# Performance work log

Measured on AMD Instinct MI355X. Metric: run time of the kernel, lower is better.

The kernel has to match this reference:

```python
import jax, jax.numpy as jnp
import numpy as np

E = 1024  # embed_dim

def setup_inputs() -> dict:
    key = jax.random.key(0)
    ks = jax.random.split(key, 7)
    s = 1.0 / np.sqrt(E)  # torch Linear default init scale (uniform bound)
    x = jax.random.normal(ks[0], (4, 2048, E), dtype=jnp.float32)
    Wq = jax.random.uniform(ks[1], (E, E), jnp.float32, -s, s)
    bq = jax.random.uniform(ks[2], (E,), jnp.float32, -s, s)
    Wk = jax.random.uniform(ks[3], (E, E), jnp.float32, -s, s)
    bk = jax.random.uniform(ks[4], (E,), jnp.float32, -s, s)
    Wv = jax.random.uniform(ks[5], (E, E), jnp.float32, -s, s)
    bv = jax.random.uniform(ks[6], (E,), jnp.float32, -s, s)
    return {"x": x, "Wq": Wq, "bq": bq, "Wk": Wk, "bk": bk, "Wv": Wv, "bv": bv}

def reference(x, Wq, bq, Wk, bk, Wv, bv):
    # torch nn.Linear: y = x @ W.T + b
    Q = jnp.einsum('bse,fe->bsf', x, Wq) + bq
    K = jnp.einsum('bse,fe->bsf', x, Wk) + bk
    V = jnp.einsum('bse,fe->bsf', x, Wv) + bv
    scale = jnp.sqrt(jnp.asarray(E, x.dtype))
    scores = jnp.einsum('bqd,bkd->bqk', Q, K) / scale  # [B,S,S]
    attn = jax.nn.softmax(scores, axis=-1)
    return jnp.einsum('bqk,bkd->bqd', attn, V)
```

## Files before the change

kernel.cpp:

```cpp
#include <hip/hip_runtime.h>
#include <hip/hip_bf16.h>


typedef __attribute__((ext_vector_type(8))) short bf16x8;
typedef __attribute__((ext_vector_type(4))) float f32x4;

#define DEVI static __device__ __forceinline__

DEVI short to_bf16(float f) {
    unsigned u = __builtin_bit_cast(unsigned, f);
    u += 0x7fffu + ((u >> 16) & 1u);
    return (short)(u >> 16);
}
DEVI float from_bf16(short s) {
    return __builtin_bit_cast(float, (unsigned)((unsigned short)s) << 16);
}

DEVI void gload_lds16(const short* g, short* l) {
    __builtin_amdgcn_global_load_lds(
        (const __attribute__((address_space(1))) void*)g,
        (__attribute__((address_space(3))) void*)l, 16, 0, 0);
}

template<int BM, int BN, int BIAS, typename TOUT>
__global__ __launch_bounds__(256, 2)
void gemm8(const short* __restrict__ A, long lda, long bsA,
           const short* __restrict__ B, long ldb, long bsB,
           const float* __restrict__ b0, const float* __restrict__ b1,
           const float* __restrict__ b2,
           TOUT* __restrict__ c0, TOUT* __restrict__ c1, TOUT* __restrict__ c2,
           long ldc, long bsC, int K, float scale)
{
    constexpr int MF = BM / 16;
    constexpr int NF = BN / 64;
    constexpr int RA = (BM * 32) / (8 * 256);
    constexpr int RB = (BN * 32) / (8 * 256);

    __shared__ __align__(16) short As[3 * BM * 32];
    __shared__ __align__(16) short Bs[3 * BN * 32];

    const int tid = threadIdx.x;
    const int z = blockIdx.z;
    const long m0 = (long)blockIdx.y * BM;
    const long n0 = (long)blockIdx.x * BN;
    const short* Ab = A + (long)z * bsA + m0 * lda;
    const short* Bb = B + (long)z * bsB + n0 * ldb;

    const int wn = tid >> 6;
    const int lane = tid & 63;
    const int lrow = lane & 15;
    const int q = lane >> 4;

    const int NT = K >> 5;

    auto stage = [&](int t, int b) {
        const long koff = (long)t * 32;
        #pragma unroll
        for (int i = 0; i < RA; ++i) {
            int s = i * 256 + tid;
            int row = s >> 2;
            int c = (s & 3) ^ ((row >> 1) & 3);
            gload_lds16(Ab + (long)row * lda + koff + c * 8,
                        &As[b * BM * 32 + s * 8]);
        }
        #pragma unroll
        for (int i = 0; i < RB; ++i) {
            int s = i * 256 + tid;
            int row = s >> 2;
            int c = (s & 3) ^ ((row >> 1) & 3);
            gload_lds16(Bb + (long)row * ldb + koff + c * 8,
                        &Bs[b * BN * 32 + s * 8]);
        }
    };

    f32x4 acc[MF][NF] = {};

    stage(0, 0);
    stage(1, 1);
    asm volatile("s_waitcnt vmcnt(6)" ::: "memory");
    __builtin_amdgcn_sched_barrier(0);
    __builtin_amdgcn_s_barrier();

    int b = 0;
    for (int t = 0; t < NT; ++t) {
        const short* Asb = &As[b * BM * 32];
        const short* Bsb = &Bs[b * BN * 32];

        bf16x8 bfr[NF];
        #pragma unroll
        for (int n = 0; n < NF; ++n) {
            int row = wn * 64 + n * 16 + lrow;
            int p = q ^ ((row >> 1) & 3);
            bfr[n] = *(const bf16x8*)&Bsb[row * 32 + p * 8];
        }
        bf16x8 af[MF];
        #pragma unroll
        for (int m = 0; m < MF; ++m) {
            int row = m * 16 + lrow;
            int p = q ^ ((row >> 1) & 3);
            af[m] = *(const bf16x8*)&Asb[row * 32 + p * 8];
        }

        if (t + 2 < NT) {
            int tb = b + 2; if (tb >= 3) tb -= 3;
            stage(t + 2, tb);
        }

        __builtin_amdgcn_s_setprio(1);
        #pragma unroll
        for (int m = 0; m < MF; ++m)
            #pragma unroll
            for (int n = 0; n < NF; ++n)
                acc[m][n] = __builtin_amdgcn_mfma_f32_16x16x32_bf16(
                    af[m], bfr[n], acc[m][n], 0, 0, 0);
        __builtin_amdgcn_s_setprio(0);

        if (t < NT - 1) {
            asm volatile("s_waitcnt lgkmcnt(0)" ::: "memory");
            asm volatile("s_waitcnt vmcnt(6)" ::: "memory");
            __builtin_amdgcn_sched_barrier(0);
            __builtin_amdgcn_s_barrier();
        }
        ++b; if (b == 3) b = 0;
    }

    const float* bias = (z == 0) ? b0 : (z == 1) ? b1 : b2;
    TOUT* Cz = ((z == 0) ? c0 : (z == 1) ? c1 : c2) + (long)z * bsC;
    TOUT* Cb = Cz + m0 * ldc + n0;
    #pragma unroll
    for (int m = 0; m < MF; ++m) {
        #pragma unroll
        for (int n = 0; n < NF; ++n) {
            #pragma unroll
            for (int r = 0; r < 4; ++r) {
                int row = m * 16 + q * 4 + r;
                int col = wn * 64 + n * 16 + lrow;
                float v = acc[m][n][r] * scale;
                if constexpr (BIAS == 1) v += bias[n0 + col];
                if constexpr (sizeof(TOUT) == 2)
                    Cb[(long)row * ldc + col] = to_bf16(v);
                else
                    Cb[(long)row * ldc + col] = v;
            }
        }
    }
}

__global__ __launch_bounds__(256)
void cvt_f32_bf16(const float* __restrict__ src, short* __restrict__ dst, int n8)
{
    int i = blockIdx.x * 256 + threadIdx.x;
    if (i < n8) {
        float4 a = ((const float4*)src)[2 * i];
        float4 b = ((const float4*)src)[2 * i + 1];
        bf16x8 o = { to_bf16(a.x), to_bf16(a.y), to_bf16(a.z), to_bf16(a.w),
                     to_bf16(b.x), to_bf16(b.y), to_bf16(b.z), to_bf16(b.w) };
        *(bf16x8*)&dst[i * 8] = o;
    }
}

__global__ __launch_bounds__(256)
void cvt3_f32_bf16(const float* __restrict__ s0, const float* __restrict__ s1,
                   const float* __restrict__ s2, short* __restrict__ dst, int n8)
{
    int zz = blockIdx.y;
    const float* src = (zz == 0) ? s0 : (zz == 1) ? s1 : s2;
    int i = blockIdx.x * 256 + threadIdx.x;
    if (i < n8) {
        float4 a = ((const float4*)src)[2 * i];
        float4 b = ((const float4*)src)[2 * i + 1];
        bf16x8 o = { to_bf16(a.x), to_bf16(a.y), to_bf16(a.z), to_bf16(a.w),
                     to_bf16(b.x), to_bf16(b.y), to_bf16(b.z), to_bf16(b.w) };
        *(bf16x8*)&dst[(long)zz * n8 * 8 + i * 8] = o;
    }
}

__global__ __launch_bounds__(256)
void softmax_rows(short* __restrict__ S, int ncols)
{
    const long row = blockIdx.x;
    short* p = S + row * (long)ncols;
    const int t = threadIdx.x;

    union { bf16x8 v; short s[8]; } u;
    u.v = *(const bf16x8*)&p[t * 8];
    float f[8];
    float m = -3.0e38f;
    #pragma unroll
    for (int j = 0; j < 8; ++j) { f[j] = from_bf16(u.s[j]); m = fmaxf(m, f[j]); }
    #pragma unroll
    for (int off = 32; off > 0; off >>= 1) m = fmaxf(m, __shfl_xor(m, off));

    __shared__ float red[8];
    const int wave = t >> 6;
    if ((t & 63) == 0) red[wave] = m;
    __syncthreads();
    m = fmaxf(fmaxf(red[0], red[1]), fmaxf(red[2], red[3]));

    float sum = 0.f;
    #pragma unroll
    for (int j = 0; j < 8; ++j) { f[j] = __expf(f[j] - m); sum += f[j]; }
    #pragma unroll
    for (int off = 32; off > 0; off >>= 1) sum += __shfl_xor(sum, off);
    if ((t & 63) == 0) red[4 + wave] = sum;
    __syncthreads();
    sum = red[4] + red[5] + red[6] + red[7];

    const float inv = 1.0f / sum;
    #pragma unroll
    for (int j = 0; j < 8; ++j) u.s[j] = to_bf16(f[j] * inv);
    *(bf16x8*)&p[t * 8] = u.v;
}

__global__ __launch_bounds__(256)
void transpose_bf16(const short* __restrict__ src, short* __restrict__ dst, int R, int Cc)
{
    __shared__ short tl[32][33];
    const long zoff = (long)blockIdx.z * R * Cc;
    const int r0 = blockIdx.x * 32;
    const int c0 = blockIdx.y * 32;
    const int tid = threadIdx.x;
    #pragma unroll
    for (int i = 0; i < 4; ++i) {
        int qq = tid + 256 * i;
        int r = qq >> 5, c = qq & 31;
        tl[r][c] = src[zoff + (long)(r0 + r) * Cc + c0 + c];
    }
    __syncthreads();
    #pragma unroll
    for (int i = 0; i < 4; ++i) {
        int qq = tid + 256 * i;
        int r = qq >> 5, c = qq & 31;
        dst[zoff + (long)(c0 + r) * R + r0 + c] = tl[c][r];
    }
}

extern "C" void kernel_launch(void* const* d_in, const int* in_sizes, int n_in,
                              void* d_out, int out_size, void* d_ws, size_t ws_size,
                              hipStream_t stream)
{
    (void)in_sizes; (void)n_in; (void)out_size; (void)ws_size;

    const float* x  = (const float*)d_in[0];
    const float* Wq = (const float*)d_in[1];
    const float* bq = (const float*)d_in[2];
    const float* Wk = (const float*)d_in[3];
    const float* bk = (const float*)d_in[4];
    const float* Wv = (const float*)d_in[5];
    const float* bv = (const float*)d_in[6];

    const int S = 2048, E = 1024;
    const long M1 = 1024l * 1024;

    short* w  = (short*)d_ws;
    short* Q  = w;
    short* Kb = w + 8 * M1;
    short* P  = w + 16 * M1;
    short* V  = w + 16 * M1;
    float* out_ws = (float*)w;

    short* dows = (short*)d_out;
    short* xb = dows;
    short* Wb = dows + 8 * M1;
    short* VT = dows;

    dim3 blk(256);

    cvt_f32_bf16<<<dim3(4096), blk, 0, stream>>>(x, xb, (int)M1);
    cvt3_f32_bf16<<<dim3(512, 3), blk, 0, stream>>>(Wq, Wk, Wv, Wb, (int)(M1 / 8));

    gemm8<128, 256, 1, short><<<dim3(4, 64, 3), blk, 0, stream>>>(
        xb, E, 0, Wb, E, M1, bq, bk, bv, Q, Kb, V, E, 0, E, 1.0f);

    transpose_bf16<<<dim3(S / 32, E / 32, 4), blk, 0, stream>>>(V, VT, S, E);

    gemm8<128, 256, 0, short><<<dim3(8, 16, 4), blk, 0, stream>>>(
        Q, E, 2 * M1, Kb, E, 2 * M1, nullptr, nullptr, nullptr,
        P, P, P, S, 4 * M1, E, 0.03125f);

    softmax_rows<<<dim3(4 * S), blk, 0, stream>>>(P, S);

    gemm8<128, 256, 0, float><<<dim3(4, 16, 4), blk, 0, stream>>>(
        P, S, 4 * M1, VT, S, 2 * M1, nullptr, nullptr, nullptr,
        out_ws, out_ws, out_ws, E, 2 * M1, S, 1.0f);

    hipMemcpyAsync(d_out, out_ws, 32l * 1024 * 1024,
                   hipMemcpyDeviceToDevice, stream);
}
```

Baseline: 201.7 us.

## Move GEMMs to 512-thread 256x256 tiles with phased MFMA and reordered buffers

Result: faster. 190.6 us (-5.5%).

```diff
diff --git a/kernel.cpp b/kernel.cpp
--- a/kernel.cpp
+++ b/kernel.cpp
@@ -22,19 +22,20 @@
         (__attribute__((address_space(3))) void*)l, 16, 0, 0);
 }
 
-template<int BM, int BN, int BIAS, typename TOUT>
-__global__ __launch_bounds__(256, 2)
-void gemm8(const short* __restrict__ A, long lda, long bsA,
+template<int BM, int BN, int WARPS_M, int WARPS_N, int BIAS, typename TOUT>
+__global__ __launch_bounds__(512, 2)
+void gemmP(const short* __restrict__ A, long lda, long bsA,
            const short* __restrict__ B, long ldb, long bsB,
            const float* __restrict__ b0, const float* __restrict__ b1,
            const float* __restrict__ b2,
            TOUT* __restrict__ c0, TOUT* __restrict__ c1, TOUT* __restrict__ c2,
            long ldc, long bsC, int K, float scale)
 {
-    constexpr int MF = BM / 16;
-    constexpr int NF = BN / 64;
-    constexpr int RA = (BM * 32) / (8 * 256);
-    constexpr int RB = (BN * 32) / (8 * 256);
+    constexpr int WM = BM / WARPS_M, WN = BN / WARPS_N;
+    constexpr int MF = WM / 16, NF = WN / 16;
+    constexpr int NPH = (MF * NF) / 16;
+    constexpr int PH_MF = MF / NPH;
+    constexpr int RA = BM / 128, RB = BN / 128, LT = RA + RB;
 
     __shared__ __align__(16) short As[3 * BM * 32];
     __shared__ __align__(16) short Bs[3 * BN * 32];
@@ -46,38 +47,44 @@
     const short* Ab = A + (long)z * bsA + m0 * lda;
     const short* Bb = B + (long)z * bsB + n0 * ldb;
 
-    const int wn = tid >> 6;
+    const int wv = tid >> 6;
+    const int wm = wv / WARPS_N;
+    const int wnn = wv % WARPS_N;
     const int lane = tid & 63;
     const int lrow = lane & 15;
     const int q = lane >> 4;
 
     const int NT = K >> 5;
 
-    auto stage = [&](int t, int b) {
+    auto stageA = [&](int t, int bb) {
         const long koff = (long)t * 32;
         #pragma unroll
         for (int i = 0; i < RA; ++i) {
-            int s = i * 256 + tid;
+            int s = i * 512 + tid;
             int row = s >> 2;
             int c = (s & 3) ^ ((row >> 1) & 3);
             gload_lds16(Ab + (long)row * lda + koff + c * 8,
-                        &As[b * BM * 32 + s * 8]);
-        }
+                        &As[bb * BM * 32 + s * 8]);
+        }
+    };
+    auto stageB = [&](int t, int bb) {
+        const long koff = (long)t * 32;
         #pragma unroll
         for (int i = 0; i < RB; ++i) {
-            int s = i * 256 + tid;
+            int s = i * 512 + tid;
             int row = s >> 2;
             int c = (s & 3) ^ ((row >> 1) & 3);
             gload_lds16(Bb + (long)row * ldb + koff + c * 8,
-                        &Bs[b * BN * 32 + s * 8]);
+                        &Bs[bb * BN * 32 + s * 8]);
         }
     };
 
     f32x4 acc[MF][NF] = {};
 
-    stage(0, 0);
-    stage(1, 1);
-    asm volatile("s_waitcnt vmcnt(6)" ::: "memory");
+    stageA(0, 0); stageB(0, 0);
+    stageA(1, 1); stageB(1, 1);
+    if constexpr (LT == 3) asm volatile("s_waitcnt vmcnt(3)" ::: "memory");
+    else                   asm volatile("s_waitcnt vmcnt(4)" ::: "memory");
     __builtin_amdgcn_sched_barrier(0);
     __builtin_amdgcn_s_barrier();
 
@@ -85,39 +92,53 @@
     for (int t = 0; t < NT; ++t) {
         const short* Asb = &As[b * BM * 32];
         const short* Bsb = &Bs[b * BN * 32];
+        int b2 = b + 2; if (b2 >= 3) b2 -= 3;
+        const bool pre = (t + 2 < NT);
 
         bf16x8 bfr[NF];
         #pragma unroll
-        for (int n = 0; n < NF; ++n) {
-            int row = wn * 64 + n * 16 + lrow;
-            int p = q ^ ((row >> 1) & 3);
-            bfr[n] = *(const bf16x8*)&Bsb[row * 32 + p * 8];
-        }
-        bf16x8 af[MF];
-        #pragma unroll
-        for (int m = 0; m < MF; ++m) {
-            int row = m * 16 + lrow;
-            int p = q ^ ((row >> 1) & 3);
-            af[m] = *(const bf16x8*)&Asb[row * 32 + p * 8];
-        }
-
-        if (t + 2 < NT) {
-            int tb = b + 2; if (tb >= 3) tb -= 3;
-            stage(t + 2, tb);
-        }
-
-        __builtin_amdgcn_s_setprio(1);
-        #pragma unroll
-        for (int m = 0; m < MF; ++m)
+        for (int p = 0; p < NPH; ++p) {
+            if (p == 0) {
+                #pragma unroll
+                for (int n = 0; n < NF; ++n) {
+                    int row = wnn * WN + n * 16 + lrow;
+                    int c = q ^ ((row >> 1) & 3);
+                    bfr[n] = *(const bf16x8*)&Bsb[row * 32 + c * 8];
+                }
+            }
+            bf16x8 af[PH_MF];
             #pragma unroll
-            for (int n = 0; n < NF; ++n)
-                acc[m][n] = __builtin_amdgcn_mfma_f32_16x16x32_bf16(
-                    af[m], bfr[n], acc[m][n], 0, 0, 0);
-        __builtin_amdgcn_s_setprio(0);
+            for (int m = 0; m < PH_MF; ++m) {
+                int row = wm * WM + (p * PH_MF + m) * 16 + lrow;
+                int c = q ^ ((row >> 1) & 3);
+                af[m] = *(const bf16x8*)&Asb[row * 32 + c * 8];
+            }
+            if (pre) {
+                if (p == 0) stageA(t + 2, b2);
+                if (p == NPH - 1) stageB(t + 2, b2);
+            }
+            __builtin_amdgcn_s_barrier();
+            asm volatile("s_waitcnt lgkmcnt(0)" ::: "memory");
+            __builtin_amdgcn_sched_barrier(0);
+            __builtin_amdgcn_s_setprio(1);
+            #pragma unroll
+            for (int m = 0; m < PH_MF; ++m)
+                #pragma unroll
+                for (int n = 0; n < NF; ++n)
+                    acc[p * PH_MF + m][n] =
+                        __builtin_amdgcn_mfma_f32_16x16x32_bf16(
+                            af[m], bfr[n], acc[p * PH_MF + m][n], 0, 0, 0);
+            __builtin_amdgcn_s_setprio(0);
+            if (p < NPH - 1) __builtin_amdgcn_s_barrier();
+        }
 
         if (t < NT - 1) {
-            asm volatile("s_waitcnt lgkmcnt(0)" ::: "memory");
-            asm volatile("s_waitcnt vmcnt(6)" ::: "memory");
+            if (pre) {
+                if constexpr (LT == 3) asm volatile("s_waitcnt vmcnt(3)" ::: "memory");
+                else                   asm volatile("s_waitcnt vmcnt(4)" ::: "memory");
+            } else {
+                asm volatile("s_waitcnt vmcnt(0)" ::: "memory");
+            }
             __builtin_amdgcn_sched_barrier(0);
             __builtin_amdgcn_s_barrier();
         }
@@ -133,8 +154,8 @@
         for (int n = 0; n < NF; ++n) {
             #pragma unroll
             for (int r = 0; r < 4; ++r) {
-                int row = m * 16 + q * 4 + r;
-                int col = wn * 64 + n * 16 + lrow;
+                int row = wm * WM + m * 16 + q * 4 + r;
+                int col = wnn * WN + n * 16 + lrow;
                 float v = acc[m][n][r] * scale;
                 if constexpr (BIAS == 1) v += bias[n0 + col];
                 if constexpr (sizeof(TOUT) == 2)
@@ -248,6 +269,7 @@
     const float* bk = (const float*)d_in[4];
     const float* Wv = (const float*)d_in[5];
     const float* bv = (const float*)d_in[6];
+    float* out = (float*)d_out;
 
     const int S = 2048, E = 1024;
     const long M1 = 1024l * 1024;
@@ -256,34 +278,34 @@
     short* Q  = w;
     short* Kb = w + 8 * M1;
     short* P  = w + 16 * M1;
-    short* V  = w + 16 * M1;
-    float* out_ws = (float*)w;
+    short* V  = w;
+    short* VT = w + 8 * M1;
 
     short* dows = (short*)d_out;
     short* xb = dows;
     short* Wb = dows + 8 * M1;
-    short* VT = dows;
-
-    dim3 blk(256);
+
+    dim3 blk(256), blkg(512);
 
     cvt_f32_bf16<<<dim3(4096), blk, 0, stream>>>(x, xb, (int)M1);
     cvt3_f32_bf16<<<dim3(512, 3), blk, 0, stream>>>(Wq, Wk, Wv, Wb, (int)(M1 / 8));
 
-    gemm8<128, 256, 1, short><<<dim3(4, 64, 3), blk, 0, stream>>>(
-        xb, E, 0, Wb, E, M1, bq, bk, bv, Q, Kb, V, E, 0, E, 1.0f);
-
-    transpose_bf16<<<dim3(S / 32, E / 32, 4), blk, 0, stream>>>(V, VT, S, E);
-
-    gemm8<128, 256, 0, short><<<dim3(8, 16, 4), blk, 0, stream>>>(
+    gemmP<256, 256, 2, 4, 1, short><<<dim3(4, 32, 2), blkg, 0, stream>>>(
+        xb, E, 0, Wb, E, M1, bq, bk, nullptr, Q, Kb, nullptr, E, 0, E, 1.0f);
+
+    gemmP<256, 256, 2, 4, 0, short><<<dim3(8, 8, 4), blkg, 0, stream>>>(
         Q, E, 2 * M1, Kb, E, 2 * M1, nullptr, nullptr, nullptr,
         P, P, P, S, 4 * M1, E, 0.03125f);
 
+    gemmP<128, 256, 2, 4, 1, short><<<dim3(4, 64, 1), blkg, 0, stream>>>(
+        xb, E, 0, Wb + 2 * M1, E, 0, bv, nullptr, nullptr,
+        V, nullptr, nullptr, E, 0, E, 1.0f);
+
+    transpose_bf16<<<dim3(S / 32, E / 32, 4), blk, 0, stream>>>(V, VT, S, E);
+
     softmax_rows<<<dim3(4 * S), blk, 0, stream>>>(P, S);
 
-    gemm8<128, 256, 0, float><<<dim3(4, 16, 4), blk, 0, stream>>>(
+    gemmP<128, 256, 2, 4, 0, float><<<dim3(4, 16, 4), blkg, 0, stream>>>(
         P, S, 4 * M1, VT, S, 2 * M1, nullptr, nullptr, nullptr,
-        out_ws, out_ws, out_ws, E, 2 * M1, S, 1.0f);
-
-    hipMemcpyAsync(d_out, out_ws, 32l * 1024 * 1024,
-                   hipMemcpyDeviceToDevice, stream);
-}
+        out, out, out, E, 2 * M1, S, 1.0f);
+}
```

## Rewrite GEMM as 512-thread 256x128 tile kernel and drop final output copy

Applied to the files above, without the earlier changes.

Measured after the change: 225.0 us. 11.5% more time.

```diff
diff --git a/kernel.cpp b/kernel.cpp
--- a/kernel.cpp
+++ b/kernel.cpp
@@ -22,119 +22,148 @@
         (__attribute__((address_space(3))) void*)l, 16, 0, 0);
 }
 
-template<int BM, int BN, int BIAS, typename TOUT>
-__global__ __launch_bounds__(256, 2)
-void gemm8(const short* __restrict__ A, long lda, long bsA,
+template<int BIAS, typename TOUT>
+__global__ __launch_bounds__(512, 2)
+void gemmW(const short* __restrict__ A, long lda, long bsA,
            const short* __restrict__ B, long ldb, long bsB,
-           const float* __restrict__ b0, const float* __restrict__ b1,
-           const float* __restrict__ b2,
+           const float* __restrict__ bi0, const float* __restrict__ bi1,
+           const float* __restrict__ bi2,
            TOUT* __restrict__ c0, TOUT* __restrict__ c1, TOUT* __restrict__ c2,
-           long ldc, long bsC, int K, float scale)
-{
-    constexpr int MF = BM / 16;
-    constexpr int NF = BN / 64;
-    constexpr int RA = (BM * 32) / (8 * 256);
-    constexpr int RB = (BN * 32) / (8 * 256);
-
-    __shared__ __align__(16) short As[3 * BM * 32];
-    __shared__ __align__(16) short Bs[3 * BN * 32];
+           long ldc, long bsC, int K, float scale, int gx)
+{
+    __shared__ __align__(16) short As[3 * 16384];
+    __shared__ __align__(16) short Bs[3 * 8192];
 
     const int tid = threadIdx.x;
-    const int z = blockIdx.z;
-    const long m0 = (long)blockIdx.y * BM;
-    const long n0 = (long)blockIdx.x * BN;
+    const int z = blockIdx.y;
+
+    const int nwg = gridDim.x;
+    const int id = blockIdx.x;
+    const int id2 = (id & 7) * (nwg >> 3) + (id >> 3);
+    const long m0 = (long)(id2 / gx) * 256;
+    const long n0 = (long)(id2 % gx) * 128;
+
     const short* Ab = A + (long)z * bsA + m0 * lda;
     const short* Bb = B + (long)z * bsB + n0 * ldb;
 
-    const int wn = tid >> 6;
+    const int wv = tid >> 6;
+    const int wm = wv >> 2;
+    const int wn = wv & 3;
     const int lane = tid & 63;
     const int lrow = lane & 15;
     const int q = lane >> 4;
 
-    const int NT = K >> 5;
-
-    auto stage = [&](int t, int b) {
-        const long koff = (long)t * 32;
-        #pragma unroll
-        for (int i = 0; i < RA; ++i) {
-            int s = i * 256 + tid;
-            int row = s >> 2;
-            int c = (s & 3) ^ ((row >> 1) & 3);
-            gload_lds16(Ab + (long)row * lda + koff + c * 8,
-                        &As[b * BM * 32 + s * 8]);
-        }
-        #pragma unroll
-        for (int i = 0; i < RB; ++i) {
-            int s = i * 256 + tid;
-            int row = s >> 2;
-            int c = (s & 3) ^ ((row >> 1) & 3);
-            gload_lds16(Bb + (long)row * ldb + koff + c * 8,
-                        &Bs[b * BN * 32 + s * 8]);
-        }
-    };
-
-    f32x4 acc[MF][NF] = {};
-
-    stage(0, 0);
-    stage(1, 1);
+    const int NT = K >> 6;
+
+    auto stA = [&](int t, int bb, int h) {
+        const long k0 = (long)t * 64;
+        #pragma unroll
+        for (int i = 0; i < 2; ++i) {
+            int s = i * 512 + tid;
+            int row = s >> 3, cc = s & 7;
+            int src = cc ^ (row & 7);
+            gload_lds16(Ab + (long)(h * 128 + row) * lda + k0 + src * 8,
+                        &As[bb * 16384 + h * 8192 + s * 8]);
+        }
+    };
+    auto stB = [&](int t, int bb) {
+        const long k0 = (long)t * 64;
+        #pragma unroll
+        for (int i = 0; i < 2; ++i) {
+            int s = i * 512 + tid;
+            int row = s >> 3, cc = s & 7;
+            int src = cc ^ (row & 7);
+            gload_lds16(Bb + (long)row * ldb + k0 + src * 8,
+                        &Bs[bb * 8192 + s * 8]);
+        }
+    };
+
+    auto ldA = [&](bf16x8 (&dst)[4][2], int bb, int half) {
+        #pragma unroll
+        for (int m = 0; m < 4; ++m) {
+            #pragma unroll
+            for (int kk = 0; kk < 2; ++kk) {
+                int rl = (half * 4 + m) * 16 + lrow;
+                int ch = (kk * 4 + q) ^ (rl & 7);
+                dst[m][kk] = *(const bf16x8*)
+                    &As[bb * 16384 + wm * 8192 + rl * 64 + ch * 8];
+            }
+        }
+    };
+    auto ldB = [&](bf16x8 (&dst)[2][2], int bb) {
+        #pragma unroll
+        for (int n = 0; n < 2; ++n) {
+            #pragma unroll
+            for (int kk = 0; kk < 2; ++kk) {
+                int rb = wn * 32 + n * 16 + lrow;
+                int ch = (kk * 4 + q) ^ (rb & 7);
+                dst[n][kk] = *(const bf16x8*)&Bs[bb * 8192 + rb * 64 + ch * 8];
+            }
+        }
+    };
+
+    f32x4 acc[8][2] = {};
+    bf16x8 afA[4][2], afB[4][2], bfE[2][2], bfO[2][2];
+
+    auto mm = [&](bf16x8 (&af)[4][2], bf16x8 (&bf)[2][2], int half) {
+        __builtin_amdgcn_s_setprio(1);
+        #pragma unroll
+        for (int m = 0; m < 4; ++m)
+            #pragma unroll
+            for (int n = 0; n < 2; ++n)
+                #pragma unroll
+                for (int kk = 0; kk < 2; ++kk)
+                    acc[half * 4 + m][n] = __builtin_amdgcn_mfma_f32_16x16x32_bf16(
+                        af[m][kk], bf[n][kk], acc[half * 4 + m][n], 0, 0, 0);
+        __builtin_amdgcn_s_setprio(0);
+    };
+
+    auto tile = [&](int t, int bb0, int bb1, int bb2,
+                    bf16x8 (&bfU)[2][2], bf16x8 (&bfL)[2][2]) {
+        const bool pre2 = (t + 2 < NT), pre1 = (t + 1 < NT);
+        asm volatile("s_waitcnt lgkmcnt(0)" ::: "memory");
+        __builtin_amdgcn_sched_barrier(0);
+        if (pre2) { stA(t + 2, bb2, 0); stB(t + 2, bb2); }
+        ldA(afB, bb0, 1);
+        mm(afA, bfU, 0);
+        asm volatile("s_waitcnt lgkmcnt(0)" ::: "memory");
+        __builtin_amdgcn_sched_barrier(0);
+        if (pre2) asm volatile("s_waitcnt vmcnt(4)" ::: "memory");
+        else      asm volatile("s_waitcnt vmcnt(0)" ::: "memory");
+        __builtin_amdgcn_sched_barrier(0);
+        __builtin_amdgcn_s_barrier();
+        if (pre2) stA(t + 2, bb2, 1);
+        if (pre1) { ldA(afA, bb1, 0); ldB(bfL, bb1); }
+        mm(afB, bfU, 1);
+    };
+
+    stA(0, 0, 0); stB(0, 0); stA(0, 0, 1);
+    stA(1, 1, 0); stB(1, 1); stA(1, 1, 1);
     asm volatile("s_waitcnt vmcnt(6)" ::: "memory");
     __builtin_amdgcn_sched_barrier(0);
     __builtin_amdgcn_s_barrier();
+    ldA(afA, 0, 0); ldB(bfE, 0);
 
     int b = 0;
-    for (int t = 0; t < NT; ++t) {
-        const short* Asb = &As[b * BM * 32];
-        const short* Bsb = &Bs[b * BN * 32];
-
-        bf16x8 bfr[NF];
-        #pragma unroll
-        for (int n = 0; n < NF; ++n) {
-            int row = wn * 64 + n * 16 + lrow;
-            int p = q ^ ((row >> 1) & 3);
-            bfr[n] = *(const bf16x8*)&Bsb[row * 32 + p * 8];
-        }
-        bf16x8 af[MF];
-        #pragma unroll
-        for (int m = 0; m < MF; ++m) {
-            int row = m * 16 + lrow;
-            int p = q ^ ((row >> 1) & 3);
-            af[m] = *(const bf16x8*)&Asb[row * 32 + p * 8];
-        }
-
-        if (t + 2 < NT) {
-            int tb = b + 2; if (tb >= 3) tb -= 3;
-            stage(t + 2, tb);
-        }
-
-        __builtin_amdgcn_s_setprio(1);
-        #pragma unroll
-        for (int m = 0; m < MF; ++m)
-            #pragma unroll
-            for (int n = 0; n < NF; ++n)
-                acc[m][n] = __builtin_amdgcn_mfma_f32_16x16x32_bf16(
-                    af[m], bfr[n], acc[m][n], 0, 0, 0);
-        __builtin_amdgcn_s_setprio(0);
-
-        if (t < NT - 1) {
-            asm volatile("s_waitcnt lgkmcnt(0)" ::: "memory");
-            asm volatile("s_waitcnt vmcnt(6)" ::: "memory");
-            __builtin_amdgcn_sched_barrier(0);
-            __builtin_amdgcn_s_barrier();
-        }
-        ++b; if (b == 3) b = 0;
-    }
-
-    const float* bias = (z == 0) ? b0 : (z == 1) ? b1 : b2;
-    TOUT* Cz = ((z == 0) ? c0 : (z == 1) ? c1 : c2) + (long)z * bsC;
-    TOUT* Cb = Cz + m0 * ldc + n0;
-    #pragma unroll
-    for (int m = 0; m < MF; ++m) {
-        #pragma unroll
-        for (int n = 0; n < NF; ++n) {
+    for (int t = 0; t < NT; t += 2) {
+        int B1 = b + 1; if (B1 >= 3) B1 -= 3;
+        int B2 = b + 2; if (B2 >= 3) B2 -= 3;
+        tile(t,     b,  B1, B2, bfE, bfO);
+        tile(t + 1, B1, B2, b,  bfO, bfE);
+        b += 2; if (b >= 3) b -= 3;
+    }
+
+    const float* bias = (z == 0) ? bi0 : (z == 1) ? bi1 : bi2;
+    TOUT* Cb = (((z == 0) ? c0 : (z == 1) ? c1 : c2) + (long)z * bsC)
+               + m0 * ldc + n0;
+    #pragma unroll
+    for (int m = 0; m < 8; ++m) {
+        #pragma unroll
+        for (int n = 0; n < 2; ++n) {
             #pragma unroll
             for (int r = 0; r < 4; ++r) {
-                int row = m * 16 + q * 4 + r;
-                int col = wn * 64 + n * 16 + lrow;
+                int row = wm * 128 + m * 16 + q * 4 + r;
+                int col = wn * 32 + n * 16 + lrow;
                 float v = acc[m][n][r] * scale;
                 if constexpr (BIAS == 1) v += bias[n0 + col];
                 if constexpr (sizeof(TOUT) == 2)
@@ -248,6 +277,7 @@
     const float* bk = (const float*)d_in[4];
     const float* Wv = (const float*)d_in[5];
     const float* bv = (const float*)d_in[6];
+    float* out = (float*)d_out;
 
     const int S = 2048, E = 1024;
     const long M1 = 1024l * 1024;
@@ -256,34 +286,35 @@
     short* Q  = w;
     short* Kb = w + 8 * M1;
     short* P  = w + 16 * M1;
-    short* V  = w + 16 * M1;
-    float* out_ws = (float*)w;
+    short* V  = w;
+    short* VT = w + 8 * M1;
 
     short* dows = (short*)d_out;
     short* xb = dows;
     short* Wb = dows + 8 * M1;
-    short* VT = dows;
-
-    dim3 blk(256);
+
+    dim3 blk(256), blkg(512);
 
     cvt_f32_bf16<<<dim3(4096), blk, 0, stream>>>(x, xb, (int)M1);
     cvt3_f32_bf16<<<dim3(512, 3), blk, 0, stream>>>(Wq, Wk, Wv, Wb, (int)(M1 / 8));
 
-    gemm8<128, 256, 1, short><<<dim3(4, 64, 3), blk, 0, stream>>>(
-        xb, E, 0, Wb, E, M1, bq, bk, bv, Q, Kb, V, E, 0, E, 1.0f);
+    gemmW<1, short><<<dim3(256, 2), blkg, 0, stream>>>(
+        xb, E, 0, Wb, E, M1, bq, bk, nullptr,
+        Q, Kb, nullptr, E, 0, E, 1.0f, 8);
+
+    gemmW<0, short><<<dim3(128, 4), blkg, 0, stream>>>(
+        Q, E, 2 * M1, Kb, E, 2 * M1, nullptr, nullptr, nullptr,
+        P, P, P, S, 4 * M1, E, 0.03125f, 16);
+
+    gemmW<1, short><<<dim3(256, 1), blkg, 0, stream>>>(
+        xb, E, 0, Wb + 2 * M1, E, 0, bv, nullptr, nullptr,
+        V, nullptr, nullptr, E, 0, E, 1.0f, 8);
 
     transpose_bf16<<<dim3(S / 32, E / 32, 4), blk, 0, stream>>>(V, VT, S, E);
 
-    gemm8<128, 256, 0, short><<<dim3(8, 16, 4), blk, 0, stream>>>(
-        Q, E, 2 * M1, Kb, E, 2 * M1, nullptr, nullptr, nullptr,
-        P, P, P, S, 4 * M1, E, 0.03125f);
-
     softmax_rows<<<dim3(4 * S), blk, 0, stream>>>(P, S);
 
-    gemm8<128, 256, 0, float><<<dim3(4, 16, 4), blk, 0, stream>>>(
+    gemmW<0, float><<<dim3(64, 4), blkg, 0, stream>>>(
         P, S, 4 * M1, VT, S, 2 * M1, nullptr, nullptr, nullptr,
-        out_ws, out_ws, out_ws, E, 2 * M1, S, 1.0f);
-
-    hipMemcpyAsync(d_out, out_ws, 32l * 1024 * 1024,
-                   hipMemcpyDeviceToDevice, stream);
-}
+        out, out, out, E, 2 * M1, S, 1.0f, 8);
+}
```

## Compute V transposed directly via GEMM and write output in place

Applied to the files above, without the earlier changes.

Measured after the change: 187.0 us. 7.3% less time.

```diff
diff --git a/kernel.cpp b/kernel.cpp
--- a/kernel.cpp
+++ b/kernel.cpp
@@ -124,7 +124,8 @@
         ++b; if (b == 3) b = 0;
     }
 
-    const float* bias = (z == 0) ? b0 : (z == 1) ? b1 : b2;
+    const float* bias = (BIAS == 2) ? b0
+                      : ((z == 0) ? b0 : (z == 1) ? b1 : b2);
     TOUT* Cz = ((z == 0) ? c0 : (z == 1) ? c1 : c2) + (long)z * bsC;
     TOUT* Cb = Cz + m0 * ldc + n0;
     #pragma unroll
@@ -137,6 +138,7 @@
                 int col = wn * 64 + n * 16 + lrow;
                 float v = acc[m][n][r] * scale;
                 if constexpr (BIAS == 1) v += bias[n0 + col];
+                if constexpr (BIAS == 2) v += bias[m0 + row];
                 if constexpr (sizeof(TOUT) == 2)
                     Cb[(long)row * ldc + col] = to_bf16(v);
                 else
@@ -212,29 +214,6 @@
     *(bf16x8*)&p[t * 8] = u.v;
 }
 
-__global__ __launch_bounds__(256)
-void transpose_bf16(const short* __restrict__ src, short* __restrict__ dst, int R, int Cc)
-{
-    __shared__ short tl[32][33];
-    const long zoff = (long)blockIdx.z * R * Cc;
-    const int r0 = blockIdx.x * 32;
-    const int c0 = blockIdx.y * 32;
-    const int tid = threadIdx.x;
-    #pragma unroll
-    for (int i = 0; i < 4; ++i) {
-        int qq = tid + 256 * i;
-        int r = qq >> 5, c = qq & 31;
-        tl[r][c] = src[zoff + (long)(r0 + r) * Cc + c0 + c];
-    }
-    __syncthreads();
-    #pragma unroll
-    for (int i = 0; i < 4; ++i) {
-        int qq = tid + 256 * i;
-        int r = qq >> 5, c = qq & 31;
-        dst[zoff + (long)(c0 + r) * R + r0 + c] = tl[c][r];
-    }
-}
-
 extern "C" void kernel_launch(void* const* d_in, const int* in_sizes, int n_in,
                               void* d_out, int out_size, void* d_ws, size_t ws_size,
                               hipStream_t stream)
@@ -248,6 +227,7 @@
     const float* bk = (const float*)d_in[4];
     const float* Wv = (const float*)d_in[5];
     const float* bv = (const float*)d_in[6];
+    float* out = (float*)d_out;
 
     const int S = 2048, E = 1024;
     const long M1 = 1024l * 1024;
@@ -256,34 +236,31 @@
     short* Q  = w;
     short* Kb = w + 8 * M1;
     short* P  = w + 16 * M1;
-    short* V  = w + 16 * M1;
-    float* out_ws = (float*)w;
+    short* VT = w + 8 * M1;
 
     short* dows = (short*)d_out;
     short* xb = dows;
     short* Wb = dows + 8 * M1;
-    short* VT = dows;
 
     dim3 blk(256);
 
     cvt_f32_bf16<<<dim3(4096), blk, 0, stream>>>(x, xb, (int)M1);
     cvt3_f32_bf16<<<dim3(512, 3), blk, 0, stream>>>(Wq, Wk, Wv, Wb, (int)(M1 / 8));
 
-    gemm8<128, 256, 1, short><<<dim3(4, 64, 3), blk, 0, stream>>>(
-        xb, E, 0, Wb, E, M1, bq, bk, bv, Q, Kb, V, E, 0, E, 1.0f);
-
-    transpose_bf16<<<dim3(S / 32, E / 32, 4), blk, 0, stream>>>(V, VT, S, E);
+    gemm8<128, 256, 1, short><<<dim3(4, 64, 2), blk, 0, stream>>>(
+        xb, E, 0, Wb, E, M1, bq, bk, nullptr, Q, Kb, nullptr, E, 0, E, 1.0f);
 
     gemm8<128, 256, 0, short><<<dim3(8, 16, 4), blk, 0, stream>>>(
         Q, E, 2 * M1, Kb, E, 2 * M1, nullptr, nullptr, nullptr,
         P, P, P, S, 4 * M1, E, 0.03125f);
 
+    gemm8<128, 256, 2, short><<<dim3(8, 8, 4), blk, 0, stream>>>(
+        Wb + 2 * M1, E, 0, xb, E, 2 * M1, bv, nullptr, nullptr,
+        VT, VT, VT, S, 2 * M1, E, 1.0f);
+
     softmax_rows<<<dim3(4 * S), blk, 0, stream>>>(P, S);
 
     gemm8<128, 256, 0, float><<<dim3(4, 16, 4), blk, 0, stream>>>(
         P, S, 4 * M1, VT, S, 2 * M1, nullptr, nullptr, nullptr,
-        out_ws, out_ws, out_ws, E, 2 * M1, S, 1.0f);
-
-    hipMemcpyAsync(d_out, out_ws, 32l * 1024 * 1024,
-                   hipMemcpyDeviceToDevice, stream);
-}
+        out, out, out, E, 2 * M1, S, 1.0f);
+}
```
